# Optimization experiments

Measured on AMD Instinct MI355X. Metric: run time of the kernel, lower is better.

## Reference

```python
import jax, jax.numpy as jnp
import numpy as np

N, T, I, H = 256, 256, 512, 512

def setup_inputs() -> dict:
    key = jax.random.key(0)
    ks = jax.random.split(key, 9)
    s = 1.0 / np.sqrt(H)  # torch GRUCell init scale
    x = jax.random.normal(ks[0], (N, T, I), jnp.float32)
    is_init = jax.random.bernoulli(ks[1], 0.05, (N, T))  # bool resets
    hx = jax.random.normal(ks[2], (N, T, H), jnp.float32)
    W_ih = jax.random.uniform(ks[3], (3 * H, I), jnp.float32, -s, s)
    W_hh = jax.random.uniform(ks[4], (3 * H, H), jnp.float32, -s, s)
    b_ih = jax.random.uniform(ks[5], (3 * H,), jnp.float32, -s, s)
    b_hh = jax.random.uniform(ks[6], (3 * H,), jnp.float32, -s, s)
    W_out = jax.random.uniform(ks[7], (H, H), jnp.float32, -s, s)
    b_out = jax.random.uniform(ks[8], (H,), jnp.float32, -s, s)
    return {"x": x, "hx": hx, "W_ih": W_ih, "W_hh": W_hh, "b_ih": b_ih,
            "b_hh": b_hh, "W_out": W_out, "b_out": b_out, "is_init": is_init}

def _gru_forward(x, hx, W_ih, W_hh, b_ih, b_hh, W_out, b_out, is_init):
    # recurrent_mode branch; learnable_init=False -> reset to zeros
    mask = is_init[..., None]                         # [N,T,1] bool
    h0 = jnp.where(mask[:, 0], 0.0, hx[:, 0])        # [N,H]
    # precompute input-to-hidden gates for all steps: [N,T,3H]
    xi = jnp.einsum('nti,gi->ntg', x, W_ih) + b_ih

    def step(h, inp):
        xi_t, m_t = inp                              # [N,3H], [N,1]
        h = jnp.where(m_t, 0.0, h)                   # per-step init masking
        hh = h @ W_hh.T + b_hh                       # [N,3H]
        xr, xz, xn = jnp.split(xi_t, 3, axis=-1)
        hr, hz, hn = jnp.split(hh, 3, axis=-1)
        r = jax.nn.sigmoid(xr + hr)
        z = jax.nn.sigmoid(xz + hz)
        n = jnp.tanh(xn + r * hn)
        h_new = (1.0 - z) * n + z * h
        return h_new, h_new

    hT, hs = jax.lax.scan(step, h0,
                          (xi.transpose(1, 0, 2), mask.transpose(1, 0, 2)))
    hs = hs.transpose(1, 0, 2)                       # [N,T,H]
    output = hs @ W_out.T + b_out                    # LazyLinear projection
    hx_out = jnp.broadcast_to(hT[:, None, :], (hT.shape[0], T, hT.shape[1]))
    return output, hx_out

def reference(x, hx, W_ih, W_hh, b_ih, b_hh, W_out, b_out, is_init):
    return _gru_forward(x, hx, W_ih, W_hh, b_ih, b_hh, W_out, b_out, is_init)
```

## Files before the change

kernel.cpp:

```cpp
#include <hip/hip_runtime.h>

#define NB 256
#define TT 256
#define II 512
#define HH 512
#define GG 1536

typedef unsigned short ushort_t;
typedef unsigned int uint_t;
typedef unsigned long long ull_t;
typedef __attribute__((ext_vector_type(8))) short short8;
typedef __attribute__((ext_vector_type(4))) float f32x4;

typedef __attribute__((address_space(3))) void lds_void;
typedef const __attribute__((address_space(1))) void glb_void;

__device__ __forceinline__ ushort_t f2bf(float f) {
  union { float f; unsigned int u; } x; x.f = f;
  unsigned int r = x.u + 0x7FFFu + ((x.u >> 16) & 1u);
  return (ushort_t)(r >> 16);
}
__device__ __forceinline__ float bf2f(ushort_t b) {
  union { unsigned int u; float f; } x; x.u = ((unsigned int)b) << 16;
  return x.f;
}
__device__ __forceinline__ float sigmoidf_(float x) {
  return __fdividef(1.0f, 1.0f + __expf(-x));
}
__device__ __forceinline__ float tanhf_(float x) {
  float t = __expf(2.0f * x);
  return 1.0f - __fdividef(2.0f, t + 1.0f);
}
__device__ __forceinline__ short8 pack8(float4 a, float4 b) {
  short8 r;
  r[0] = (short)f2bf(a.x); r[1] = (short)f2bf(a.y);
  r[2] = (short)f2bf(a.z); r[3] = (short)f2bf(a.w);
  r[4] = (short)f2bf(b.x); r[5] = (short)f2bf(b.y);
  r[6] = (short)f2bf(b.z); r[7] = (short)f2bf(b.w);
  return r;
}

__global__ void mask_detect_kernel(const unsigned char* __restrict__ src,
                                   unsigned char* __restrict__ mask8) {
  __shared__ int fByte, fOdd;
  const int tid = threadIdx.x;
  if (tid == 0) { fByte = 0; fOdd = 0; }
  __syncthreads();
  const uint_t* w = (const uint_t*)src;
  int ab = 0, ao = 0;
  for (int i = tid; i < NB * TT; i += blockDim.x) {
    if ((i & 3) == 1 && src[i]) ab = 1;
    if (i < 16384 && (i & 1) == 1 && w[i]) ao = 1;
  }
  if (ab) fByte = 1;
  if (ao) fOdd = 1;
  __syncthreads();
  const int isByte = fByte, isW32 = fOdd;
  for (int i = tid; i < NB * TT; i += blockDim.x) {
    unsigned char m;
    if (isByte)      m = src[i] ? 1 : 0;
    else if (isW32)  m = w[i] ? 1 : 0;
    else             m = w[2 * i] ? 1 : 0;
    mask8[i] = m;
  }
}

__global__ void cvt_f2bf(const float* __restrict__ src, ushort_t* __restrict__ dst,
                         int n4) {
  int stride = gridDim.x * blockDim.x;
  for (int i = blockIdx.x * blockDim.x + threadIdx.x; i < n4; i += stride) {
    const float4 v = reinterpret_cast<const float4*>(src)[i];
    ushort4 o;
    o.x = f2bf(v.x); o.y = f2bf(v.y); o.z = f2bf(v.z); o.w = f2bf(v.w);
    reinterpret_cast<ushort4*>(dst)[i] = o;
  }
}

__global__ void pack_whh(const float* __restrict__ W, ushort_t* __restrict__ out) {
  int idx = blockIdx.x * blockDim.x + threadIdx.x;
  if (idx >= 96 * 16 * 64) return;
  int l = idx & 63;
  int tk = idx >> 6;
  int tile = tk >> 4, kk = tk & 15;
  int row = tile * 16 + (l & 15);
  int k = kk * 32 + (l >> 4) * 8;
  const float* s = W + (size_t)row * HH + k;
  short8 v;
#pragma unroll
  for (int e = 0; e < 8; ++e) v[e] = (short)f2bf(s[e]);
  *reinterpret_cast<short8*>(out + (size_t)idx * 8) = v;
}

template <int AF32, int CF32>
__global__ __launch_bounds__(256) void gemm_bt(
    const void* __restrict__ Av, const ushort_t* __restrict__ B,
    const float* __restrict__ bias, void* __restrict__ Cv, int NC) {
  __shared__ ushort_t As[128 * 32];
  __shared__ ushort_t Bs[128 * 32];
  const int tid = threadIdx.x;
  const int lane = tid & 63;
  const int w = tid >> 6;
  const int wr = w >> 1, wc = w & 1;
  const int c15 = lane & 15, l4 = lane >> 4;
  const int mbase = blockIdx.x * 128;
  const int nbase = blockIdx.y * 128;

  const int rs = tid >> 2;
  const int kb = (tid & 3) * 8;

  f32x4 acc[4][4] = {};

  const float4* Bg = reinterpret_cast<const float4*>(B);
  auto bIdx = [&](int c, int kt) {
    return ((size_t)(nbase + rs + 64 * c) * 512 + kt * 32 + kb) >> 3;
  };
  float4 rb0 = Bg[bIdx(0, 0)], rb1 = Bg[bIdx(1, 0)];

  const float4* Agf = reinterpret_cast<const float4*>(Av);
  auto aEl = [&](int c, int kt) {
    return (size_t)(mbase + rs + 64 * c) * 512 + kt * 32 + kb;
  };
  float4 a0a, a0b, a1a, a1b;
  float4 h0, h1;
  if constexpr (AF32) {
    a0a = Agf[aEl(0, 0) >> 2]; a0b = Agf[(aEl(0, 0) >> 2) + 1];
    a1a = Agf[aEl(1, 0) >> 2]; a1b = Agf[(aEl(1, 0) >> 2) + 1];
  } else {
    h0 = Agf[aEl(0, 0) >> 3];
    h1 = Agf[aEl(1, 0) >> 3];
  }

  for (int kt = 0; kt < 16; ++kt) {
    __syncthreads();
    if constexpr (AF32) {
      *reinterpret_cast<short8*>(&As[(size_t)tid * 8]) = pack8(a0a, a0b);
      *reinterpret_cast<short8*>(&As[(size_t)(tid + 256) * 8]) = pack8(a1a, a1b);
    } else {
      reinterpret_cast<float4*>(As)[tid] = h0;
      reinterpret_cast<float4*>(As)[tid + 256] = h1;
    }
    reinterpret_cast<float4*>(Bs)[tid] = rb0;
    reinterpret_cast<float4*>(Bs)[tid + 256] = rb1;
    if (kt < 15) {
      if constexpr (AF32) {
        a0a = Agf[aEl(0, kt + 1) >> 2]; a0b = Agf[(aEl(0, kt + 1) >> 2) + 1];
        a1a = Agf[aEl(1, kt + 1) >> 2]; a1b = Agf[(aEl(1, kt + 1) >> 2) + 1];
      } else {
        h0 = Agf[aEl(0, kt + 1) >> 3];
        h1 = Agf[aEl(1, kt + 1) >> 3];
      }
      rb0 = Bg[bIdx(0, kt + 1)]; rb1 = Bg[bIdx(1, kt + 1)];
    }
    __syncthreads();
    short8 af[4], bq[4];
#pragma unroll
    for (int m = 0; m < 4; ++m)
      af[m] = *reinterpret_cast<const short8*>(&As[(wr * 64 + m * 16 + c15) * 32 + l4 * 8]);
#pragma unroll
    for (int n = 0; n < 4; ++n)
      bq[n] = *reinterpret_cast<const short8*>(&Bs[(wc * 64 + n * 16 + c15) * 32 + l4 * 8]);
#pragma unroll
    for (int m = 0; m < 4; ++m)
#pragma unroll
      for (int n = 0; n < 4; ++n)
        acc[m][n] = __builtin_amdgcn_mfma_f32_16x16x32_bf16(af[m], bq[n], acc[m][n], 0, 0, 0);
  }

#pragma unroll
  for (int n = 0; n < 4; ++n) {
    const int col = nbase + wc * 64 + n * 16 + c15;
    const float bv = bias[col];
#pragma unroll
    for (int m = 0; m < 4; ++m) {
      const int row = mbase + wr * 64 + m * 16 + l4 * 4;
#pragma unroll
      for (int q = 0; q < 4; ++q) {
        const float v = acc[m][n][q] + bv;
        if constexpr (CF32)
          reinterpret_cast<float*>(Cv)[(size_t)(row + q) * NC + col] = v;
        else
          reinterpret_cast<ushort_t*>(Cv)[(size_t)(row + q) * NC + col] = f2bf(v);
      }
    }
  }
}

__global__ __launch_bounds__(256, 1) void gru_rec(
    const ushort_t* __restrict__ xi, const ushort_t* __restrict__ Wpk,
    const float* __restrict__ hx, const float* __restrict__ bhh,
    const unsigned char* __restrict__ mask8,
    ushort_t* __restrict__ hs, float* __restrict__ hT,
    char* __restrict__ xch) {
  extern __shared__ ushort_t smem[];
  const int HAF_U = 32768, XIL_U = 49152;

  const int tid = threadIdx.x;
  const int lane = tid & 63;
  const int w = tid >> 6;
  const int c15 = lane & 15, l4 = lane >> 4;
  const int bid = blockIdx.x;
  const int a = bid & 7;
  const int b = bid >> 3;
  const int n0 = b * 16;

  const int jl = w * 16 + c15;
  const int jfull = a * 64 + jl;
  const float br = bhh[jfull], bz = bhh[512 + jfull], bn = bhh[1024 + jfull];

#pragma unroll
  for (int kk = 0; kk < 16; ++kk)
    __builtin_amdgcn_global_load_lds(
        (glb_void*)(Wpk + ((size_t)((32 + a * 4 + w) * 16 + kk)) * 512 + lane * 8),
        (lds_void*)(smem + w * 8192 + kk * 512 + lane * 8), 16, 0, 0);

  const int wbr = ((0 * 32 + a * 4 + w) * 16) * 512 + lane * 8;
  const int wbn = ((2 * 32 + a * 4 + w) * 16) * 512 + lane * 8;
  short8 wr_[16], wn_[16];
#pragma unroll
  for (int kk = 0; kk < 16; ++kk) {
    wr_[kk] = *(const short8*)(Wpk + wbr + kk * 512);
    wn_[kk] = *(const short8*)(Wpk + wbn + kk * 512);
  }

  size_t xg0, xg1 = 0;
  {
    int c = tid, s = c / 24, r = c % 24, g = r >> 3, p = r & 7;
    xg0 = ((size_t)(n0 + s) * TT) * GG + g * 512 + a * 64 + p * 8;
    if (tid < 128) {
      c = tid + 256; s = c / 24; r = c % 24; g = r >> 3; p = r & 7;
      xg1 = ((size_t)(n0 + s) * TT) * GG + g * 512 + a * 64 + p * 8;
    }
  }
  const int xl0 = tid * 8, xl1 = (tid + 256) * 8;

  char* slot0 = xch + (size_t)(b * 2) * 32768;
  char* slot1 = xch + (size_t)(b * 2 + 1) * 32768;

  const bool evenlane = ((c15 & 1) == 0);
  auto ubOff = [&](int s, int j) {
    return (j >> 5) * 1024 + (s + 16 * ((j & 31) >> 3)) * 16 + (j & 7) * 2;
  };

  auto pubfill = [&](char* slot, uint_t tag, int pp, const ushort_t* hb) {
    const uint_t u01 = (uint_t)hb[0] | ((uint_t)hb[1] << 16);
    const uint_t u23 = (uint_t)hb[2] | ((uint_t)hb[3] << 16);
    const uint_t p01 = __shfl_xor(u01, 1);
    const uint_t p23 = __shfl_xor(u23, 1);
    if (evenlane) {
      char* hafB = (char*)(smem + HAF_U + pp * 8192);
#pragma unroll
      for (int q = 0; q < 4; ++q) {
        const int s = l4 * 4 + q;
        const uint_t own = ((q < 2 ? u01 : u23) >> ((q & 1) * 16)) & 0xFFFFu;
        const uint_t prt = ((q < 2 ? p01 : p23) >> ((q & 1) * 16)) & 0xFFFFu;
        const int ub = ubOff(s, jfull);
        *(uint_t*)(hafB + ub) = own | (prt << 16);
        const ull_t wv = ((ull_t)((own << 16) | tag)) |
                         (((ull_t)((prt << 16) | tag)) << 32);
        __hip_atomic_store((ull_t*)(slot + (size_t)ub * 2), wv,
                           __ATOMIC_RELAXED, __HIP_MEMORY_SCOPE_AGENT);
      }
    }
  };

  float h[4];
  ushort_t hb0[4];
#pragma unroll
  for (int q = 0; q < 4; ++q) {
    const int s = l4 * 4 + q;
    const bool mk0 = mask8[(size_t)(n0 + s) * TT] != 0;
    const float v = mk0 ? 0.0f : hx[((size_t)(n0 + s) * TT) * HH + jfull];
    h[q] = v;
    hb0[q] = f2bf(v);
  }
  pubfill(slot0, 1u, 0, hb0);

  for (int t = 0; t < TT; ++t) {
    ushort_t* xb = smem + XIL_U + (t & 1) * 3072;
    __builtin_amdgcn_global_load_lds((glb_void*)(xi + xg0 + (size_t)t * GG),
                                     (lds_void*)(xb + xl0), 16, 0, 0);
    if (tid < 128)
      __builtin_amdgcn_global_load_lds((glb_void*)(xi + xg1 + (size_t)t * GG),
                                       (lds_void*)(xb + xl1), 16, 0, 0);

    const char* src = (t & 1) ? slot1 : slot0;
    const uint_t tgt = (uint_t)(t + 1);
    ull_t v[16];
    bool ok;
    do {
      ok = true;
#pragma unroll
      for (int i = 0; i < 16; ++i)
        v[i] = __hip_atomic_load((const ull_t*)(src + ((size_t)(tid + i * 256)) * 8),
                                 __ATOMIC_RELAXED, __HIP_MEMORY_SCOPE_AGENT);
#pragma unroll
      for (int i = 0; i < 16; ++i)
        if ((i >> 1) != a)
          ok &= (((uint_t)v[i] & 0xFFFFu) == tgt) &&
                (((uint_t)(v[i] >> 32) & 0xFFFFu) == tgt);
    } while (!ok);
    char* hafB = (char*)(smem + HAF_U + (t & 1) * 8192);
#pragma unroll
    for (int i = 0; i < 16; ++i)
      if ((i >> 1) != a) {
        const uint_t lo = (uint_t)(v[i] >> 16) & 0xFFFFu;
        const uint_t hi = (uint_t)(v[i] >> 48);
        *(uint_t*)(hafB + ((size_t)(tid + i * 256)) * 4) = lo | (hi << 16);
      }

    const bool domask = (t + 1 < TT);
    const int tn = domask ? (t + 1) : t;
    unsigned char mkv[4];
#pragma unroll
    for (int q = 0; q < 4; ++q)
      mkv[q] = mask8[(size_t)(n0 + l4 * 4 + q) * TT + tn];

    __syncthreads();

    short8 af[16];
#pragma unroll
    for (int kk = 0; kk < 16; ++kk)
      af[kk] = *(const short8*)(hafB + kk * 1024 + lane * 16);

    f32x4 a0 = {0.f, 0.f, 0.f, 0.f}, a1 = a0, a2 = a0;
#pragma unroll
    for (int kk = 0; kk < 16; ++kk) {
      const short8 wz = *(const short8*)(smem + w * 8192 + kk * 512 + lane * 8);
      a0 = __builtin_amdgcn_mfma_f32_16x16x32_bf16(af[kk], wr_[kk], a0, 0, 0, 0);
      a1 = __builtin_amdgcn_mfma_f32_16x16x32_bf16(af[kk], wz, a1, 0, 0, 0);
      a2 = __builtin_amdgcn_mfma_f32_16x16x32_bf16(af[kk], wn_[kk], a2, 0, 0, 0);
    }

    ushort_t hbp[4], hsv[4];
#pragma unroll
    for (int q = 0; q < 4; ++q) {
      const int s = l4 * 4 + q;
      const float xr = bf2f(xb[s * 192 + jl]);
      const float xz = bf2f(xb[s * 192 + 64 + jl]);
      const float xn = bf2f(xb[s * 192 + 128 + jl]);
      const float rr = sigmoidf_(xr + a0[q] + br);
      const float zz = sigmoidf_(xz + a1[q] + bz);
      const float nn = tanhf_(xn + rr * (a2[q] + bn));
      const float hnew = (1.0f - zz) * nn + zz * h[q];
      hsv[q] = f2bf(hnew);
      const float hp = (domask && mkv[q]) ? 0.0f : hnew;
      h[q] = hp;
      hbp[q] = f2bf(hp);
    }
    if (domask)
      pubfill(((t + 1) & 1) ? slot1 : slot0, (uint_t)(t + 2), (t + 1) & 1, hbp);
#pragma unroll
    for (int q = 0; q < 4; ++q)
      __builtin_nontemporal_store(
          hsv[q], &hs[((size_t)(n0 + l4 * 4 + q) * TT + t) * HH + jfull]);
  }

#pragma unroll
  for (int q = 0; q < 4; ++q)
    hT[(size_t)(n0 + l4 * 4 + q) * HH + jfull] = h[q];
}

__global__ void bcast_hT(const float* __restrict__ hT, float* __restrict__ dst) {
  const float4* s = (const float4*)hT;
  float4* d = (float4*)dst;
  const int total = NB * TT * HH / 4;
  const int stride = gridDim.x * blockDim.x;
  for (int c = blockIdx.x * blockDim.x + threadIdx.x; c < total; c += stride) {
    int n = c >> 15;
    int j4 = c & 127;
    d[c] = s[(n << 7) | j4];
  }
}

extern "C" void kernel_launch(void* const* d_in, const int* in_sizes, int n_in,
                              void* d_out, int out_size, void* d_ws, size_t ws_size,
                              hipStream_t stream) {
  const float* x    = (const float*)d_in[0];
  const float* hx   = (const float*)d_in[1];
  const float* Wih  = (const float*)d_in[2];
  const float* Whh  = (const float*)d_in[3];
  const float* bih  = (const float*)d_in[4];
  const float* bhh  = (const float*)d_in[5];
  const float* Wout = (const float*)d_in[6];
  const float* bout = (const float*)d_in[7];
  const unsigned char* isinit = (const unsigned char*)d_in[8];

  char* ws = (char*)d_ws;
  ushort_t* xi    = (ushort_t*)(ws);
  ushort_t* wihb  = (ushort_t*)(ws + 201326592);
  ushort_t* whhp  = (ushort_t*)(ws + 202899456);
  ushort_t* woutb = (ushort_t*)(ws + 204472320);
  unsigned char* mask8 = (unsigned char*)(ws + 204996608);
  float*    hTbuf = (float*)(ws + 205062144);
  char*     xch   = (char*)(ws + 205602816);

  float* out1 = (float*)d_out;
  float* out2 = out1 + (size_t)NB * TT * HH;
  ushort_t* hsb = (ushort_t*)out2;

  hipMemsetAsync(xch, 0, 1 << 20, stream);
  mask_detect_kernel<<<1, 1024, 0, stream>>>(isinit, mask8);
  cvt_f2bf<<<768, 256, 0, stream>>>(Wih, wihb, GG * II / 4);
  cvt_f2bf<<<256, 256, 0, stream>>>(Wout, woutb, HH * HH / 4);
  pack_whh<<<384, 256, 0, stream>>>(Whh, whhp);

  dim3 g1(512, 12);
  gemm_bt<1, 0><<<g1, 256, 0, stream>>>((const void*)x, wihb, bih, (void*)xi, GG);

  gru_rec<<<128, 256, 110592, stream>>>(xi, whhp, hx, bhh, mask8, hsb, hTbuf,
                                        xch);

  dim3 g3(512, 4);
  gemm_bt<0, 1><<<g3, 256, 0, stream>>>((const void*)hsb, woutb, bout, (void*)out1, HH);

  bcast_hT<<<2048, 256, 0, stream>>>(hTbuf, out2);
}
```

Measured before the change: 1.392 ms.

## Replace tagged-data polling with per-step arrival counters for hidden-state exchange

```diff
diff --git a/kernel.cpp b/kernel.cpp
--- a/kernel.cpp
+++ b/kernel.cpp
@@ -233,15 +233,16 @@
   }
   const int xl0 = tid * 8, xl1 = (tid + 256) * 8;
 
-  char* slot0 = xch + (size_t)(b * 2) * 32768;
-  char* slot1 = xch + (size_t)(b * 2 + 1) * 32768;
+  char* slot0 = xch + (size_t)(b * 2) * 16384;
+  char* slot1 = xch + (size_t)(b * 2 + 1) * 16384;
+  uint_t* cnt = (uint_t*)(xch + 524288) + b * 256;
 
   const bool evenlane = ((c15 & 1) == 0);
   auto ubOff = [&](int s, int j) {
     return (j >> 5) * 1024 + (s + 16 * ((j & 31) >> 3)) * 16 + (j & 7) * 2;
   };
 
-  auto pubfill = [&](char* slot, uint_t tag, int pp, const ushort_t* hb) {
+  auto pubfill = [&](char* slot, int pp, const ushort_t* hb) {
     const uint_t u01 = (uint_t)hb[0] | ((uint_t)hb[1] << 16);
     const uint_t u23 = (uint_t)hb[2] | ((uint_t)hb[3] << 16);
     const uint_t p01 = __shfl_xor(u01, 1);
@@ -254,10 +255,9 @@
         const uint_t own = ((q < 2 ? u01 : u23) >> ((q & 1) * 16)) & 0xFFFFu;
         const uint_t prt = ((q < 2 ? p01 : p23) >> ((q & 1) * 16)) & 0xFFFFu;
         const int ub = ubOff(s, jfull);
-        *(uint_t*)(hafB + ub) = own | (prt << 16);
-        const ull_t wv = ((ull_t)((own << 16) | tag)) |
-                         (((ull_t)((prt << 16) | tag)) << 32);
-        __hip_atomic_store((ull_t*)(slot + (size_t)ub * 2), wv,
+        const uint_t word = own | (prt << 16);
+        *(uint_t*)(hafB + ub) = word;
+        __hip_atomic_store((uint_t*)(slot + ub), word,
                            __ATOMIC_RELAXED, __HIP_MEMORY_SCOPE_AGENT);
       }
     }
@@ -273,7 +273,11 @@
     h[q] = v;
     hb0[q] = f2bf(v);
   }
-  pubfill(slot0, 1u, 0, hb0);
+  pubfill(slot0, 0, hb0);
+  __syncthreads();
+  if (tid == 0)
+    __hip_atomic_fetch_add(&cnt[0], 1u, __ATOMIC_RELAXED,
+                           __HIP_MEMORY_SCOPE_AGENT);
 
   for (int t = 0; t < TT; ++t) {
     ushort_t* xb = smem + XIL_U + (t & 1) * 3072;
@@ -283,30 +287,22 @@
       __builtin_amdgcn_global_load_lds((glb_void*)(xi + xg1 + (size_t)t * GG),
                                        (lds_void*)(xb + xl1), 16, 0, 0);
 
+    if (tid == 0)
+      while (__hip_atomic_load(&cnt[t], __ATOMIC_RELAXED,
+                               __HIP_MEMORY_SCOPE_AGENT) < 8u) {}
+    __syncthreads();
+
     const char* src = (t & 1) ? slot1 : slot0;
-    const uint_t tgt = (uint_t)(t + 1);
-    ull_t v[16];
-    bool ok;
-    do {
-      ok = true;
-#pragma unroll
-      for (int i = 0; i < 16; ++i)
-        v[i] = __hip_atomic_load((const ull_t*)(src + ((size_t)(tid + i * 256)) * 8),
-                                 __ATOMIC_RELAXED, __HIP_MEMORY_SCOPE_AGENT);
-#pragma unroll
-      for (int i = 0; i < 16; ++i)
-        if ((i >> 1) != a)
-          ok &= (((uint_t)v[i] & 0xFFFFu) == tgt) &&
-                (((uint_t)(v[i] >> 32) & 0xFFFFu) == tgt);
-    } while (!ok);
     char* hafB = (char*)(smem + HAF_U + (t & 1) * 8192);
 #pragma unroll
-    for (int i = 0; i < 16; ++i)
-      if ((i >> 1) != a) {
-        const uint_t lo = (uint_t)(v[i] >> 16) & 0xFFFFu;
-        const uint_t hi = (uint_t)(v[i] >> 48);
-        *(uint_t*)(hafB + ((size_t)(tid + i * 256)) * 4) = lo | (hi << 16);
-      }
+    for (int i = 0; i < 8; ++i) {
+      if (i == a) continue;
+      const size_t off = ((size_t)(tid + i * 256)) * 8;
+      const ull_t v = __hip_atomic_load((const ull_t*)(src + off),
+                                        __ATOMIC_RELAXED,
+                                        __HIP_MEMORY_SCOPE_AGENT);
+      *(ull_t*)(hafB + off) = v;
+    }
 
     const bool domask = (t + 1 < TT);
     const int tn = domask ? (t + 1) : t;
@@ -347,12 +343,22 @@
       h[q] = hp;
       hbp[q] = f2bf(hp);
     }
-    if (domask)
-      pubfill(((t + 1) & 1) ? slot1 : slot0, (uint_t)(t + 2), (t + 1) & 1, hbp);
-#pragma unroll
-    for (int q = 0; q < 4; ++q)
-      __builtin_nontemporal_store(
-          hsv[q], &hs[((size_t)(n0 + l4 * 4 + q) * TT + t) * HH + jfull]);
+    if (domask) {
+      pubfill(((t + 1) & 1) ? slot1 : slot0, (t + 1) & 1, hbp);
+#pragma unroll
+      for (int q = 0; q < 4; ++q)
+        __builtin_nontemporal_store(
+            hsv[q], &hs[((size_t)(n0 + l4 * 4 + q) * TT + t) * HH + jfull]);
+      __syncthreads();
+      if (tid == 0)
+        __hip_atomic_fetch_add(&cnt[t + 1], 1u, __ATOMIC_RELAXED,
+                               __HIP_MEMORY_SCOPE_AGENT);
+    } else {
+#pragma unroll
+      for (int q = 0; q < 4; ++q)
+        __builtin_nontemporal_store(
+            hsv[q], &hs[((size_t)(n0 + l4 * 4 + q) * TT + t) * HH + jfull]);
+    }
   }
 
 #pragma unroll
```

After: 1.496 ms. +7.4%, slower.
